# Kernel optimization log

Hardware: AMD Instinct MI355X
Metric: run time of the kernel (lower is better)

## Reference

```python
import jax, jax.numpy as jnp
import numpy as np

B, L = 2, 5            # batches (scenes) and cavs per scene (fixed record_len)
THRESHOLD = 0.01       # communication threshold (eval path)
K_SIZE, SIGMA = 5, 1.0 # fixed gaussian smoothing filter


def _gaussian_kernel():
    c = K_SIZE // 2
    xx, yy = np.mgrid[0 - c:K_SIZE - c, 0 - c:K_SIZE - c]
    k = 1.0 / (2.0 * np.pi * SIGMA) * np.exp(-(np.square(xx) + np.square(yy)) / (2.0 * SIGMA ** 2))
    return jnp.asarray(k, jnp.float32)[None, None]  # OIHW (1,1,k,k)


def setup_inputs() -> dict:
    key = jax.random.key(0)
    ks = jax.random.split(key, 9)
    N, C, H, W, A = B * L, 64, 128, 256, 2
    return {
        "x": jax.random.normal(ks[0], (N, C, H, W), jnp.float32),
        "psm_single": jax.random.normal(ks[1], (N, A, H, W), jnp.float32),
        "inv_delay": jax.random.uniform(ks[2], (N,), jnp.float32, 0.1, 5.0),
        "ew_w": jax.random.normal(ks[3], (1,), jnp.float32),
        "ew_b": jax.random.normal(ks[4], (1,), jnp.float32),
        "ewc_w": jax.random.normal(ks[5], (1,), jnp.float32),
        "ewc_b": jax.random.normal(ks[6], (1,), jnp.float32),
        "sta_w1": jax.random.normal(ks[7], (4, 64), jnp.float32) * 0.1,
        "sta_w2": jax.random.normal(ks[8], (64, 4), jnp.float32) * 0.1,
    }


def reference(x, psm_single, inv_delay, ew_w, ew_b, ewc_w, ewc_b, sta_w1, sta_w2):
    N, C, H, W = x.shape
    dt = x.dtype

    # EnhanceWeight: per-cav AoI gate tanh(fc(1/(delay+0.1))) + 1
    enw = jnp.tanh(inv_delay * ew_w[0] + ew_b[0]) + 1.0          # (N,)
    x = x * enw[:, None, None, None]

    # Communication: sigmoid confidence, max over anchors, AoI gate, gaussian smooth
    conf = jax.nn.sigmoid(psm_single).max(axis=1, keepdims=True)  # (N,1,H,W)
    enc = jnp.tanh(inv_delay * ewc_w[0] + ewc_b[0]) + 1.0
    conf = conf * enc[:, None, None, None]
    conf = jax.lax.conv_general_dilated(
        conf, _gaussian_kernel().astype(dt), (1, 1), 'SAME',
        dimension_numbers=('NCHW', 'OIHW', 'NCHW'))
    mask = (conf > THRESHOLD).astype(dt)                          # (N,1,H,W)
    mask = mask.reshape(B, L, 1, H, W).at[:, 0].set(1.0)          # ego always communicates
    comm_rate = mask.mean()

    xm = x.reshape(B, L, C, H, W) * mask                          # masked per-cav features

    # TransformerFusion: per-pixel cross-agent attention, keep ego (row 0) output only
    feats = xm.transpose(0, 3, 4, 1, 2).reshape(B, H * W, L, C)   # (B, P, L, C)
    scale = 1.0 / jnp.sqrt(jnp.asarray(C, dt))
    scores = jnp.einsum('bpc,bplc->bpl', feats[:, :, 0], feats) * scale
    attn = jax.nn.softmax(scores, axis=-1)                        # (B, P, L)
    fused = jnp.einsum('bpl,bplc->bpc', attn, feats)              # (B, P, C)
    x_fuse = fused.transpose(0, 2, 1).reshape(B, C, H, W)

    # ShortTermAttention: channel gate from shared MLP over avg- and max-pooled stats
    def fc(v):  # v: (B, C)
        return jax.nn.relu(v @ sta_w1.T) @ sta_w2.T

    avg = x_fuse.mean(axis=(2, 3))
    mx = x_fuse.max(axis=(2, 3))
    gate = jax.nn.sigmoid(fc(avg) + fc(mx))                       # (B, C)
    out = x_fuse * gate[:, :, None, None]
    return out, comm_rate
```

## Files before the change

kernel.cpp:

```cpp
#include <hip/hip_runtime.h>
#include <math.h>

#define BB 2
#define LL 5
#define NN 10
#define CC 64
#define HH 128
#define WW 256
#define PP (HH*WW)
#define NP (NN*PP)


__global__ __launch_bounds__(256) void k_confmask(const float* __restrict__ psm,
                                                  const float* __restrict__ inv_delay,
                                                  const float* __restrict__ ewc_w,
                                                  const float* __restrict__ ewc_b,
                                                  float* __restrict__ mask,
                                                  float* __restrict__ cntp) {
    const float g0 = 0.15915494309189535f;
    const float g1 = 0.09653235263005391f;
    const float g2 = 0.05854983152431917f;
    const float g4 = 0.02153927930184936f;
    const float g5 = 0.01306423328468446f;
    const float g8 = 0.00291502449738744f;
    const float G[25] = { g8,g5,g4,g5,g8,
                          g5,g2,g1,g2,g5,
                          g4,g1,g0,g1,g4,
                          g5,g2,g1,g2,g5,
                          g8,g5,g4,g5,g8 };
    int blk = blockIdx.x;
    int n   = blk >> 7;
    int h   = blk & 127;
    int t   = threadIdx.x;
    float enc = tanhf(inv_delay[n] * ewc_w[0] + ewc_b[0]) + 1.0f;
    const float* pn0 = psm + (n * 2 + 0) * PP;
    const float* pn1 = psm + (n * 2 + 1) * PP;

    __shared__ float cs[5][WW];
#pragma unroll
    for (int r = 0; r < 5; ++r) {
        int row = h - 2 + r;
        float v = 0.0f;
        if ((unsigned)row < (unsigned)HH) {
            float a0 = pn0[row * WW + t];
            float a1 = pn1[row * WW + t];
            v = fmaxf(1.0f / (1.0f + expf(-a0)), 1.0f / (1.0f + expf(-a1))) * enc;
        }
        cs[r][t] = v;
    }
    __syncthreads();

    float acc = 0.0f;
#pragma unroll
    for (int r = 0; r < 5; ++r) {
#pragma unroll
        for (int dx = -2; dx <= 2; ++dx) {
            int col = t + dx;
            if ((unsigned)col < (unsigned)WW)
                acc += cs[r][col] * G[r * 5 + (dx + 2)];
        }
    }
    float mv = (acc > 0.01f) ? 1.0f : 0.0f;
    if ((n % LL) == 0) mv = 1.0f;
    mask[n * PP + h * WW + t] = mv;

    float v = mv;
#pragma unroll
    for (int o = 32; o > 0; o >>= 1) v += __shfl_down(v, o, 64);
    __shared__ float sred[4];
    int lane = t & 63, wid = t >> 6;
    if (lane == 0) sred[wid] = v;
    __syncthreads();
    if (t == 0) cntp[blk] = sred[0] + sred[1] + sred[2] + sred[3];
}

__global__ __launch_bounds__(512) void k_attnfuse(const float* __restrict__ x,
                                                  const float* __restrict__ mask,
                                                  const float* __restrict__ inv_delay,
                                                  const float* __restrict__ ew_w,
                                                  const float* __restrict__ ew_b,
                                                  float* __restrict__ out) {
    int blk = blockIdx.x;
    int b   = blk >> 9;
    int lane = threadIdx.x & 63;
    int wv   = threadIdx.x >> 6;
    int p = ((blk & 511) << 6) + lane;
    const float* xb = x + b * (LL * CC * PP) + p;
    int cbase = wv << 3;

    float xr[8][5];
    float s5[5] = {0.f, 0.f, 0.f, 0.f, 0.f};
#pragma unroll
    for (int cc = 0; cc < 8; ++cc) {
        const float* xc = xb + (cbase + cc) * PP;
#pragma unroll
        for (int l = 0; l < LL; ++l) xr[cc][l] = xc[l * CC * PP];
        float q = xr[cc][0];
#pragma unroll
        for (int l = 0; l < LL; ++l) s5[l] += q * xr[cc][l];
    }

    __shared__ float sred[8][5][64];
#pragma unroll
    for (int l = 0; l < LL; ++l) sred[wv][l][lane] = s5[l];
    __syncthreads();

    float ew0 = ew_w[0], eb0 = ew_b[0];
    float a[5];
    {
        float m[5], t[5], sc[5], e[5];
#pragma unroll
        for (int l = 0; l < LL; ++l) {
            float tl = 0.f;
#pragma unroll
            for (int w = 0; w < 8; ++w) tl += sred[w][l][lane];
            t[l] = tl;
            float en = tanhf(inv_delay[b * LL + l] * ew0 + eb0) + 1.0f;
            m[l] = en * mask[(b * LL + l) * PP + p];
        }
        const float scale = 0.125f;
#pragma unroll
        for (int l = 0; l < LL; ++l) sc[l] = t[l] * m[0] * m[l] * scale;
        float mxv = fmaxf(fmaxf(fmaxf(sc[0], sc[1]), fmaxf(sc[2], sc[3])), sc[4]);
        float sum = 0.f;
#pragma unroll
        for (int l = 0; l < LL; ++l) { e[l] = expf(sc[l] - mxv); sum += e[l]; }
        float inv = 1.0f / sum;
#pragma unroll
        for (int l = 0; l < LL; ++l) a[l] = e[l] * inv * m[l];
    }

    float* ob = out + b * (CC * PP) + p;
#pragma unroll
    for (int cc = 0; cc < 8; ++cc) {
        float f = 0.f;
#pragma unroll
        for (int l = 0; l < LL; ++l) f += a[l] * xr[cc][l];
        ob[(cbase + cc) * PP] = f;
    }
}

__global__ void k_reduce(const float* __restrict__ xfuse,
                         float* __restrict__ avg_part,
                         float* __restrict__ mx_part) {
    int blk = blockIdx.x;
    int bc = blk >> 1;
    int half = blk & 1;
    const float4* row = (const float4*)(xfuse + bc * PP) + half * 4096;
    float s = 0.0f, m = -INFINITY;
    for (int i = threadIdx.x; i < 4096; i += 256) {
        float4 v = row[i];
        s += v.x + v.y + v.z + v.w;
        m = fmaxf(m, fmaxf(fmaxf(v.x, v.y), fmaxf(v.z, v.w)));
    }
#pragma unroll
    for (int o = 32; o > 0; o >>= 1) {
        s += __shfl_down(s, o, 64);
        m = fmaxf(m, __shfl_down(m, o, 64));
    }
    __shared__ float ss[4], sm[4];
    int lane = threadIdx.x & 63, wid = threadIdx.x >> 6;
    if (lane == 0) { ss[wid] = s; sm[wid] = m; }
    __syncthreads();
    if (threadIdx.x == 0) {
        avg_part[blk] = ss[0] + ss[1] + ss[2] + ss[3];
        mx_part[blk]  = fmaxf(fmaxf(sm[0], sm[1]), fmaxf(sm[2], sm[3]));
    }
}

__global__ __launch_bounds__(256) void k_scalegate(float* __restrict__ out,
                                                   const float* __restrict__ avg_part,
                                                   const float* __restrict__ mx_part,
                                                   const float* __restrict__ w1,
                                                   const float* __restrict__ w2,
                                                   const float* __restrict__ cntp) {
    int idx = blockIdx.x * 256 + threadIdx.x;
    int bc = idx >> 13;
    int b  = bc >> 6;
    int c  = bc & 63;
    __shared__ float hs[4];
    if (threadIdx.x < 4) {
        int j = threadIdx.x;
        float ha = 0.f, hm = 0.f;
        const float invP = 1.0f / (float)PP;
        for (int ch = 0; ch < CC; ++ch) {
            int i = (b * CC + ch) * 2;
            float av = (avg_part[i] + avg_part[i + 1]) * invP;
            float mv = fmaxf(mx_part[i], mx_part[i + 1]);
            float wv = w1[j * CC + ch];
            ha += av * wv;
            hm += mv * wv;
        }
        hs[j] = fmaxf(ha, 0.0f) + fmaxf(hm, 0.0f);
    }
    float4 v = ((float4*)out)[idx];
    __syncthreads();
    float g = hs[0] * w2[c * 4 + 0] + hs[1] * w2[c * 4 + 1]
            + hs[2] * w2[c * 4 + 2] + hs[3] * w2[c * 4 + 3];
    float gate = 1.0f / (1.0f + expf(-g));
    v.x *= gate; v.y *= gate; v.z *= gate; v.w *= gate;
    ((float4*)out)[idx] = v;

    if (blockIdx.x == 0) {
        float s = 0.0f;
        for (int j = threadIdx.x; j < 1280; j += 256) s += cntp[j];
#pragma unroll
        for (int o = 32; o > 0; o >>= 1) s += __shfl_down(s, o, 64);
        __shared__ float cs[4];
        int lane = threadIdx.x & 63, wid = threadIdx.x >> 6;
        if (lane == 0) cs[wid] = s;
        __syncthreads();
        if (threadIdx.x == 0)
            out[BB * CC * PP] = (cs[0] + cs[1] + cs[2] + cs[3]) * (1.0f / (float)NP);
    }
}

extern "C" void kernel_launch(void* const* d_in, const int* in_sizes, int n_in,
                              void* d_out, int out_size, void* d_ws, size_t ws_size,
                              hipStream_t stream) {
    const float* x         = (const float*)d_in[0];
    const float* psm       = (const float*)d_in[1];
    const float* inv_delay = (const float*)d_in[2];
    const float* ew_w      = (const float*)d_in[3];
    const float* ew_b      = (const float*)d_in[4];
    const float* ewc_w     = (const float*)d_in[5];
    const float* ewc_b     = (const float*)d_in[6];
    const float* w1        = (const float*)d_in[7];
    const float* w2        = (const float*)d_in[8];
    float* out = (float*)d_out;
    float* wsf = (float*)d_ws;

    float* avgp = wsf + 64;
    float* mxp  = wsf + 320;
    float* cntp = wsf + 576;
    float* mask = wsf + 4096;

    k_confmask<<<NN * HH, 256, 0, stream>>>(psm, inv_delay, ewc_w, ewc_b, mask, cntp);
    k_attnfuse<<<1024, 512, 0, stream>>>(x, mask, inv_delay, ew_w, ew_b, out);
    k_reduce<<<256, 256, 0, stream>>>(out, avgp, mxp);
    k_scalegate<<<BB * CC * PP / 4 / 256, 256, 0, stream>>>(out, avgp, mxp, w1, w2, cntp);
}
```

Baseline: 53.62 us.

## Fuse confidence-mask computation into attention-fusion kernel

Removes the separate confidence/mask kernel and computes the smoothed sigmoid confidence mask inside the attention kernel, using a shared-memory halo tile of 5 cavs x 5 rows x 68 columns per block. This eliminates the mask write/read round trip through global memory and one kernel launch. The cost is that neighbouring blocks recompute overlapping halo sigmoids, and the attention kernel takes on extra shared memory and per-block work. The comm-rate partial count now comes from one wave per block, and the final reduction sums 1024 partials instead of 1280.

```diff
diff --git a/kernel.cpp b/kernel.cpp
--- a/kernel.cpp
+++ b/kernel.cpp
@@ -11,11 +11,14 @@
 #define NP (NN*PP)
 
 
-__global__ __launch_bounds__(256) void k_confmask(const float* __restrict__ psm,
+__global__ __launch_bounds__(512) void k_attnfuse(const float* __restrict__ x,
+                                                  const float* __restrict__ psm,
                                                   const float* __restrict__ inv_delay,
+                                                  const float* __restrict__ ew_w,
+                                                  const float* __restrict__ ew_b,
                                                   const float* __restrict__ ewc_w,
                                                   const float* __restrict__ ewc_b,
-                                                  float* __restrict__ mask,
+                                                  float* __restrict__ out,
                                                   float* __restrict__ cntp) {
     const float g0 = 0.15915494309189535f;
     const float g1 = 0.09653235263005391f;
@@ -28,63 +31,16 @@
                           g4,g1,g0,g1,g4,
                           g5,g2,g1,g2,g5,
                           g8,g5,g4,g5,g8 };
-    int blk = blockIdx.x;
-    int n   = blk >> 7;
-    int h   = blk & 127;
-    int t   = threadIdx.x;
-    float enc = tanhf(inv_delay[n] * ewc_w[0] + ewc_b[0]) + 1.0f;
-    const float* pn0 = psm + (n * 2 + 0) * PP;
-    const float* pn1 = psm + (n * 2 + 1) * PP;
-
-    __shared__ float cs[5][WW];
-#pragma unroll
-    for (int r = 0; r < 5; ++r) {
-        int row = h - 2 + r;
-        float v = 0.0f;
-        if ((unsigned)row < (unsigned)HH) {
-            float a0 = pn0[row * WW + t];
-            float a1 = pn1[row * WW + t];
-            v = fmaxf(1.0f / (1.0f + expf(-a0)), 1.0f / (1.0f + expf(-a1))) * enc;
-        }
-        cs[r][t] = v;
-    }
-    __syncthreads();
-
-    float acc = 0.0f;
-#pragma unroll
-    for (int r = 0; r < 5; ++r) {
-#pragma unroll
-        for (int dx = -2; dx <= 2; ++dx) {
-            int col = t + dx;
-            if ((unsigned)col < (unsigned)WW)
-                acc += cs[r][col] * G[r * 5 + (dx + 2)];
-        }
-    }
-    float mv = (acc > 0.01f) ? 1.0f : 0.0f;
-    if ((n % LL) == 0) mv = 1.0f;
-    mask[n * PP + h * WW + t] = mv;
-
-    float v = mv;
-#pragma unroll
-    for (int o = 32; o > 0; o >>= 1) v += __shfl_down(v, o, 64);
-    __shared__ float sred[4];
-    int lane = t & 63, wid = t >> 6;
-    if (lane == 0) sred[wid] = v;
-    __syncthreads();
-    if (t == 0) cntp[blk] = sred[0] + sred[1] + sred[2] + sred[3];
-}
-
-__global__ __launch_bounds__(512) void k_attnfuse(const float* __restrict__ x,
-                                                  const float* __restrict__ mask,
-                                                  const float* __restrict__ inv_delay,
-                                                  const float* __restrict__ ew_w,
-                                                  const float* __restrict__ ew_b,
-                                                  float* __restrict__ out) {
+
     int blk = blockIdx.x;
     int b   = blk >> 9;
-    int lane = threadIdx.x & 63;
-    int wv   = threadIdx.x >> 6;
-    int p = ((blk & 511) << 6) + lane;
+    int tid  = threadIdx.x;
+    int lane = tid & 63;
+    int wv   = tid >> 6;
+    int pblock = blk & 511;
+    int p  = (pblock << 6) + lane;
+    int h  = pblock >> 2;
+    int c0 = (pblock & 3) << 6;
     const float* xb = x + b * (LL * CC * PP) + p;
     int cbase = wv << 3;
 
@@ -99,11 +55,54 @@
 #pragma unroll
         for (int l = 0; l < LL; ++l) s5[l] += q * xr[cc][l];
     }
-
     __shared__ float sred[8][5][64];
 #pragma unroll
     for (int l = 0; l < LL; ++l) sred[wv][l][lane] = s5[l];
+
+    __shared__ float cs[5 * 340];
+    {
+        float encs[5];
+#pragma unroll
+        for (int l = 0; l < LL; ++l)
+            encs[l] = tanhf(inv_delay[b * LL + l] * ewc_w[0] + ewc_b[0]) + 1.0f;
+        for (int idx = tid; idx < 1700; idx += 512) {
+            int l   = idx / 340;
+            int rem = idx - l * 340;
+            int r   = rem / 68;
+            int cc2 = rem - r * 68;
+            int row = h - 2 + r;
+            int col = c0 - 2 + cc2;
+            float v = 0.0f;
+            if ((unsigned)row < (unsigned)HH && (unsigned)col < (unsigned)WW) {
+                int n = b * LL + l;
+                float a0 = psm[(n * 2 + 0) * PP + row * WW + col];
+                float a1 = psm[(n * 2 + 1) * PP + row * WW + col];
+                v = fmaxf(1.0f / (1.0f + expf(-a0)), 1.0f / (1.0f + expf(-a1))) * encs[l];
+            }
+            cs[idx] = v;
+        }
+    }
     __syncthreads();
+
+    float mv[5];
+#pragma unroll
+    for (int l = 0; l < LL; ++l) {
+        float acc = 0.0f;
+#pragma unroll
+        for (int r = 0; r < 5; ++r)
+#pragma unroll
+            for (int dx = 0; dx < 5; ++dx)
+                acc += cs[l * 340 + r * 68 + lane + dx] * G[r * 5 + dx];
+        mv[l] = (acc > 0.01f) ? 1.0f : 0.0f;
+    }
+    mv[0] = 1.0f;
+
+    if (wv == 0) {
+        float v = mv[0] + mv[1] + mv[2] + mv[3] + mv[4];
+#pragma unroll
+        for (int o = 32; o > 0; o >>= 1) v += __shfl_down(v, o, 64);
+        if (lane == 0) cntp[blk] = v;
+    }
 
     float ew0 = ew_w[0], eb0 = ew_b[0];
     float a[5];
@@ -116,7 +115,7 @@
             for (int w = 0; w < 8; ++w) tl += sred[w][l][lane];
             t[l] = tl;
             float en = tanhf(inv_delay[b * LL + l] * ew0 + eb0) + 1.0f;
-            m[l] = en * mask[(b * LL + l) * PP + p];
+            m[l] = en * mv[l];
         }
         const float scale = 0.125f;
 #pragma unroll
@@ -203,15 +202,15 @@
 
     if (blockIdx.x == 0) {
         float s = 0.0f;
-        for (int j = threadIdx.x; j < 1280; j += 256) s += cntp[j];
+        for (int j = threadIdx.x; j < 1024; j += 256) s += cntp[j];
 #pragma unroll
         for (int o = 32; o > 0; o >>= 1) s += __shfl_down(s, o, 64);
-        __shared__ float cs[4];
+        __shared__ float cs2[4];
         int lane = threadIdx.x & 63, wid = threadIdx.x >> 6;
-        if (lane == 0) cs[wid] = s;
+        if (lane == 0) cs2[wid] = s;
         __syncthreads();
         if (threadIdx.x == 0)
-            out[BB * CC * PP] = (cs[0] + cs[1] + cs[2] + cs[3]) * (1.0f / (float)NP);
+            out[BB * CC * PP] = (cs2[0] + cs2[1] + cs2[2] + cs2[3]) * (1.0f / (float)NP);
     }
 }
 
@@ -233,10 +232,9 @@
     float* avgp = wsf + 64;
     float* mxp  = wsf + 320;
     float* cntp = wsf + 576;
-    float* mask = wsf + 4096;
-
-    k_confmask<<<NN * HH, 256, 0, stream>>>(psm, inv_delay, ewc_w, ewc_b, mask, cntp);
-    k_attnfuse<<<1024, 512, 0, stream>>>(x, mask, inv_delay, ew_w, ew_b, out);
+
+    k_attnfuse<<<1024, 512, 0, stream>>>(x, psm, inv_delay, ew_w, ew_b, ewc_w, ewc_b,
+                                         out, cntp);
     k_reduce<<<256, 256, 0, stream>>>(out, avgp, mxp);
     k_scalegate<<<BB * CC * PP / 4 / 256, 256, 0, stream>>>(out, avgp, mxp, w1, w2, cntp);
 }
```

Result: slower. 55.56 us (+3.6%).
